# Kernel tuning notes

Hardware: AMD Instinct MI355X
Metric: run time of the kernel (lower is better)

Reference implementation:

```python
import jax, jax.numpy as jnp
import numpy as np

B, C, W, H = 4, 256, 128, 128
BLK = 16
D = C // 8


def setup_inputs() -> dict:
    key = jax.random.key(0)
    ks = jax.random.split(key, 7)
    s = 0.05
    return {
        "x": jax.random.normal(ks[0], (B, C, W, H), jnp.float32),
        "Wq": jax.random.normal(ks[1], (D, C), jnp.float32) * s,
        "bq": jax.random.normal(ks[2], (D,), jnp.float32) * s,
        "Wk": jax.random.normal(ks[3], (D, C), jnp.float32) * s,
        "bk": jax.random.normal(ks[4], (D,), jnp.float32) * s,
        "Wv": jax.random.normal(ks[5], (C, C), jnp.float32) * s,
        "bv": jax.random.normal(ks[6], (C,), jnp.float32) * s,
        "gamma": jnp.full((1,), 0.5, jnp.float32),
    }


def reference(x, Wq, bq, Wk, bk, Wv, bv, gamma):
    Bx, Cx, Wx, Hx = x.shape
    blk = BLK
    pw = (blk - Wx % blk) % blk
    ph = (blk - Hx % blk) % blk
    xp = jnp.pad(x, ((0, 0), (0, 0), (0, pw), (0, ph))) if (pw or ph) else x
    Wp, Hp = xp.shape[2], xp.shape[3]
    nW, nH = Wp // blk, Hp // blk
    N = blk * blk
    # partition into non-overlapping blk x blk windows -> (G, C, N)
    xb = xp.reshape(Bx, Cx, nW, blk, nH, blk).transpose(0, 2, 4, 1, 3, 5)
    xb = xb.reshape(-1, Cx, N)
    # padding mask: positions whose channel-abs-sum is zero are masked out
    mask = jnp.abs(xb).sum(axis=1) > 0  # (G, N) bool
    # 1x1 convs == per-pixel linear projections
    q = jnp.einsum('dc,gcn->gnd', Wq, xb) + bq            # (G, N, D)
    k = jnp.einsum('dc,gcn->gdn', Wk, xb) + bk[:, None]   # (G, D, N)
    energy = jnp.einsum('gnd,gdm->gnm', q, k)             # (G, N, N)
    NEG = jnp.float32(-1e9)
    energy = jnp.where(mask[:, None, :], energy, NEG)  # mask keys
    energy = jnp.where(mask[:, :, None], energy, NEG)  # mask queries
    att = jax.nn.softmax(energy, axis=-1)
    v = jnp.einsum('dc,gcn->gdn', Wv, xb) + bv[:, None]   # (G, C, N)
    out = jnp.einsum('gcm,gnm->gcn', v, att)              # (G, C, N)
    out = out.reshape(Bx, nW, nH, Cx, blk, blk).transpose(0, 3, 1, 4, 2, 5)
    out = out.reshape(Bx, Cx, Wp, Hp)[:, :, :Wx, :Hx]
    out = gamma * out + x
    return out, att
```

## Files before the change

### kernel.cpp

```cpp
#include <hip/hip_runtime.h>

typedef unsigned short u16;
typedef __attribute__((ext_vector_type(8))) short short8;
typedef __attribute__((ext_vector_type(4))) short s16x4;
typedef __attribute__((ext_vector_type(4))) float f32x4;

#define CC 256
#define WW 128
#define HH 128
#define DD 32
#define NN 256
#define WH (WW * HH)
#define P8 524288
#define OUTEL 16777216

__device__ __forceinline__ u16 f2bf(float f) {
  unsigned u = __float_as_uint(f);
  return (u16)((u + 0x7FFFu + ((u >> 16) & 1u)) >> 16);
}
__device__ __forceinline__ float bf2f(u16 h) {
  return __uint_as_float(((unsigned)h) << 16);
}

__global__ __launch_bounds__(256) void k_pack(const float* __restrict__ Wq,
                                              const float* __restrict__ Wk,
                                              float* __restrict__ wqk) {
  int idx = blockIdx.x * 256 + threadIdx.x;
  int r = idx >> 8, c = idx & 255;
  float v = (r < 32) ? Wq[r * 256 + c] : Wk[(r - 32) * 256 + c];
  wqk[c * 64 + r] = v;
}

__global__ __launch_bounds__(1024) void k_qk(const float* __restrict__ x,
                                             const float* __restrict__ wqk,
                                             const float* __restrict__ bq,
                                             const float* __restrict__ bk,
                                             u16* __restrict__ qk) {
  __shared__ float xs[2][64 * 256];
  int hw = blockIdx.x;
  int g = (hw & 7) * 32 + (hw >> 3);
  int bb = g >> 6, wb = (g >> 3) & 7, hb = g & 7;
  int w0 = wb * 16, h0 = hb * 16;
  int t = threadIdx.x, ln = t & 63;
  int dg = __builtin_amdgcn_readfirstlane(t >> 6);
  int dq4 = dg & 7, is_k = dg >> 3;
  const float* xwin = x + (size_t)bb * CC * WH + (size_t)w0 * HH + h0;

  f32x4 st[4];
#pragma unroll
  for (int j = 0; j < 4; ++j) {
    int lin = j * 1024 + t;
    int c = lin >> 6, sub = lin & 63;
    st[j] = *(const f32x4*)(xwin + (size_t)c * WH + (sub >> 2) * HH + (sub & 3) * 4);
  }
#pragma unroll
  for (int j = 0; j < 4; ++j) {
    int lin = j * 1024 + t;
    int c = lin >> 6, sub = lin & 63;
    *(f32x4*)&xs[0][c * 256 + sub * 4] = st[j];
  }

  float acc[4][4];
#pragma unroll
  for (int j = 0; j < 4; ++j)
#pragma unroll
    for (int i = 0; i < 4; ++i) acc[j][i] = 0.f;

  for (int s = 0; s < 4; ++s) {
    int nxt = s + 1;
    if (nxt < 4) {
#pragma unroll
      for (int j = 0; j < 4; ++j) {
        int lin = j * 1024 + t;
        int c = lin >> 6, sub = lin & 63;
        st[j] = *(const f32x4*)(xwin + (size_t)(nxt * 64 + c) * WH + (sub >> 2) * HH +
                                (sub & 3) * 4);
      }
    }
    __syncthreads();
    const float* xb = xs[s & 1];
    const float* wp = wqk + (s * 64) * 64 + dg * 4;
#pragma unroll 4
    for (int cc = 0; cc < 64; ++cc) {
      f32x4 xv = *(const f32x4*)(xb + cc * 256 + 4 * ln);
      f32x4 wv4 = *(const f32x4*)(wp + cc * 64);
#pragma unroll
      for (int j = 0; j < 4; ++j)
#pragma unroll
        for (int i = 0; i < 4; ++i) acc[j][i] = fmaf(wv4[j], xv[i], acc[j][i]);
    }
    if (nxt < 4) {
#pragma unroll
      for (int j = 0; j < 4; ++j) {
        int lin = j * 1024 + t;
        int c = lin >> 6, sub = lin & 63;
        *(f32x4*)&xs[nxt & 1][c * 256 + sub * 4] = st[j];
      }
    }
  }

  const float* bsrc = is_k ? bk : bq;
  float bias[4];
#pragma unroll
  for (int j = 0; j < 4; ++j) bias[j] = bsrc[dq4 * 4 + j];

  u16* ph = qk + ((size_t)((is_k << 3) + (dq4 >> 1))) * P8;
  int sub = (dq4 & 1) * 4;
#pragma unroll
  for (int i = 0; i < 4; ++i) {
    int m = 4 * ln + i;
    s16x4 hv, lv;
#pragma unroll
    for (int j = 0; j < 4; ++j) {
      float v = acc[j][i] + bias[j];
      u16 h = f2bf(v);
      hv[j] = (short)h;
      lv[j] = (short)f2bf(v - bf2f(h));
    }
    size_t ro = (size_t)(g * NN + m) * 8 + sub;
    *(s16x4*)(ph + ro) = hv;
    *(s16x4*)(ph + 4 * (size_t)P8 + ro) = lv;
  }
}

__global__ __launch_bounds__(512, 2) void k_v(const float* __restrict__ x,
                                              const float* __restrict__ Wv,
                                              const float* __restrict__ bv,
                                              u16* __restrict__ vws) {
  __shared__ u16 xb[256 * 44];
  int hw = blockIdx.x;
  int L = (hw & 7) * 64 + (hw >> 3);
  int g = L >> 1, ch = L & 1;
  int bb = g >> 6, wb = (g >> 3) & 7, hb = g & 7;
  int w0 = wb * 16, h0 = hb * 16;
  int t = threadIdx.x, ln = t & 63, wv = t >> 6;
  int cw = wv & 3, mh = wv >> 2;
  int cb = ch * 128 + cw * 32;
  int mb = mh * 128;
  const float* xg = x + (size_t)bb * CC * WH;

  f32x4 acc[2][8];
#pragma unroll
  for (int ci = 0; ci < 2; ++ci)
#pragma unroll
    for (int mt = 0; mt < 8; ++mt) acc[ci][mt] = (f32x4){0.f, 0.f, 0.f, 0.f};

  for (int ks = 0; ks < 8; ++ks) {
    int c0 = ks * 32;
    int q = ln >> 4, cl = wv * 4 + q;
#pragma unroll
    for (int it = 0; it < 4; ++it) {
      int mm = it * 64 + 4 * (ln & 15);
      f32x4 xv = *(const f32x4*)(xg + (size_t)(c0 + cl) * WH + (size_t)(w0 + (mm >> 4)) * HH +
                                 h0 + (mm & 15));
#pragma unroll
      for (int j = 0; j < 4; ++j) xb[(mm + j) * 44 + cl] = f2bf(xv[j]);
    }
    __syncthreads();

    short8 af[2];
#pragma unroll
    for (int ci = 0; ci < 2; ++ci) {
      int row = cb + ci * 16 + (ln & 15);
      const float* wp = Wv + (size_t)row * CC + c0 + (ln >> 4) * 8;
      f32x4 wa = *(const f32x4*)wp;
      f32x4 wb2 = *(const f32x4*)(wp + 4);
#pragma unroll
      for (int j = 0; j < 4; ++j) {
        af[ci][j] = (short)f2bf(wa[j]);
        af[ci][4 + j] = (short)f2bf(wb2[j]);
      }
    }
#pragma unroll
    for (int mt = 0; mt < 8; ++mt) {
      const u16* bp = &xb[(mb + mt * 16 + (ln & 15)) * 44 + (ln >> 4) * 8];
      union { short8 v; s16x4 h[2]; } bu;
      bu.h[0] = *(const s16x4*)bp;
      bu.h[1] = *(const s16x4*)(bp + 4);
#pragma unroll
      for (int ci = 0; ci < 2; ++ci)
        acc[ci][mt] = __builtin_amdgcn_mfma_f32_16x16x32_bf16(af[ci], bu.v, acc[ci][mt], 0, 0, 0);
    }
    __syncthreads();
  }

#pragma unroll
  for (int ci = 0; ci < 2; ++ci)
#pragma unroll
    for (int mt = 0; mt < 8; ++mt)
#pragma unroll
      for (int r = 0; r < 4; ++r) {
        int c = cb + ci * 16 + (ln >> 4) * 4 + r;
        int m = mb + mt * 16 + (ln & 15);
        vws[(size_t)(g * CC + c) * NN + m] = f2bf(acc[ci][mt][r] + bv[c]);
      }
}

__global__ __launch_bounds__(256, 4) void k_attn(const float* __restrict__ x,
                                                 const u16* __restrict__ qk,
                                                 const u16* __restrict__ vws,
                                                 const float* __restrict__ gamma,
                                                 float* __restrict__ dout) {
  __shared__ u16 att_lds[64 * 256];
  int hw = blockIdx.x;
  int L = (hw & 7) * 128 + (hw >> 3);
  int g = L >> 2, qt = L & 3;
  int bb = g >> 6, wb = (g >> 3) & 7, hb = g & 7;
  int w0 = wb * 16, h0 = hb * 16;
  int t = threadIdx.x, ln = t & 63, wv = t >> 6;
  float gam = gamma[0];
  float* attg = dout + (size_t)OUTEL;
  char* smem = (char*)att_lds;
  int n0 = qt * 64;
  int nt = n0 + wv * 16;
  int oct = ln >> 4;

  const u16* qb = qk + (size_t)oct * P8 + (size_t)(g * NN + nt + (ln & 15)) * 8;
  short8 ahi = *(const short8*)qb;
  short8 alo = *(const short8*)(qb + 4 * (size_t)P8);
  f32x4 e[16];
#pragma unroll
  for (int mt = 0; mt < 16; ++mt) e[mt] = (f32x4){0.f, 0.f, 0.f, 0.f};
#pragma unroll
  for (int mt = 0; mt < 16; ++mt) {
    const u16* kb = qk + (size_t)(8 + oct) * P8 + (size_t)(g * NN + mt * 16 + (ln & 15)) * 8;
    short8 bhi = *(const short8*)kb;
    short8 blo = *(const short8*)(kb + 4 * (size_t)P8);
    e[mt] = __builtin_amdgcn_mfma_f32_16x16x32_bf16(ahi, bhi, e[mt], 0, 0, 0);
    e[mt] = __builtin_amdgcn_mfma_f32_16x16x32_bf16(alo, bhi, e[mt], 0, 0, 0);
    e[mt] = __builtin_amdgcn_mfma_f32_16x16x32_bf16(ahi, blo, e[mt], 0, 0, 0);
  }

  float inv[4];
#pragma unroll
  for (int r = 0; r < 4; ++r) {
    float m0 = e[0][r];
#pragma unroll
    for (int mt = 1; mt < 16; ++mt) m0 = fmaxf(m0, e[mt][r]);
    m0 = fmaxf(m0, __shfl_xor(m0, 1));
    m0 = fmaxf(m0, __shfl_xor(m0, 2));
    m0 = fmaxf(m0, __shfl_xor(m0, 4));
    m0 = fmaxf(m0, __shfl_xor(m0, 8));
    float s = 0.f;
#pragma unroll
    for (int mt = 0; mt < 16; ++mt) {
      float p = __expf(e[mt][r] - m0);
      e[mt][r] = p;
      s += p;
    }
    s += __shfl_xor(s, 1);
    s += __shfl_xor(s, 2);
    s += __shfl_xor(s, 4);
    s += __shfl_xor(s, 8);
    inv[r] = 1.0f / s;
  }

#pragma unroll
  for (int mt = 0; mt < 16; ++mt)
#pragma unroll
    for (int r = 0; r < 4; ++r) {
      int nn = wv * 16 + (ln >> 4) * 4 + r;
      int m = mt * 16 + (ln & 15);
      int byteoff = nn * 512 + ((2 * m) ^ ((nn & 7) << 4));
      *(u16*)(smem + byteoff) = f2bf(e[mt][r] * inv[r]);
    }
  __syncthreads();

#pragma unroll
  for (int c = 0; c < 16; ++c) {
    int nn = c * 4 + (t >> 6);
    int m0 = 4 * (t & 63);
    int byteoff = nn * 512 + ((2 * m0) ^ ((nn & 7) << 4));
    s16x4 bv4 = *(const s16x4*)(smem + byteoff);
    f32x4 fv;
#pragma unroll
    for (int j = 0; j < 4; ++j) fv[j] = bf2f((u16)bv4[j]);
    *(f32x4*)(attg + (size_t)(g * NN + n0 + nn) * NN + m0) = fv;
  }

  int cbase = wv * 64;
  f32x4 o[4][4];
#pragma unroll
  for (int ci = 0; ci < 4; ++ci)
#pragma unroll
    for (int ni = 0; ni < 4; ++ni) o[ci][ni] = (f32x4){0.f, 0.f, 0.f, 0.f};

#pragma unroll
  for (int k = 0; k < 8; ++k) {
    short8 a[4];
#pragma unroll
    for (int ci = 0; ci < 4; ++ci)
      a[ci] = *(const short8*)&vws[(size_t)(g * CC + cbase + ci * 16 + (ln & 15)) * NN + k * 32 +
                                   (ln >> 4) * 8];
    short8 bf[4];
#pragma unroll
    for (int ni = 0; ni < 4; ++ni) {
      int nn = ni * 16 + (ln & 15);
      int byteoff = nn * 512 + ((2 * (k * 32 + (ln >> 4) * 8)) ^ ((nn & 7) << 4));
      bf[ni] = *(const short8*)(smem + byteoff);
    }
#pragma unroll
    for (int ci = 0; ci < 4; ++ci)
#pragma unroll
      for (int ni = 0; ni < 4; ++ni)
        o[ci][ni] = __builtin_amdgcn_mfma_f32_16x16x32_bf16(a[ci], bf[ni], o[ci][ni], 0, 0, 0);
  }

#pragma unroll
  for (int ci = 0; ci < 4; ++ci)
#pragma unroll
    for (int ni = 0; ni < 4; ++ni)
#pragma unroll
      for (int r = 0; r < 4; ++r) {
        int c = cbase + ci * 16 + (ln >> 4) * 4 + r;
        int n = n0 + ni * 16 + (ln & 15);
        size_t addr = (size_t)(bb * CC + c) * WH + (size_t)(w0 + (n >> 4)) * HH + h0 + (n & 15);
        dout[addr] = gam * o[ci][ni][r] + x[addr];
      }
}

extern "C" void kernel_launch(void* const* d_in, const int* in_sizes, int n_in,
                              void* d_out, int out_size, void* d_ws, size_t ws_size,
                              hipStream_t stream) {
  const float* x = (const float*)d_in[0];
  const float* Wq = (const float*)d_in[1];
  const float* bq = (const float*)d_in[2];
  const float* Wk = (const float*)d_in[3];
  const float* bk = (const float*)d_in[4];
  const float* Wv = (const float*)d_in[5];
  const float* bv = (const float*)d_in[6];
  const float* gamma = (const float*)d_in[7];
  float* out = (float*)d_out;

  float* wqk = (float*)d_ws;
  u16* qk = (u16*)((char*)d_ws + 65536);
  u16* vws = qk + 16 * (size_t)P8;

  k_pack<<<64, 256, 0, stream>>>(Wq, Wk, wqk);
  k_qk<<<256, 1024, 0, stream>>>(x, wqk, bq, bk, qk);
  k_v<<<512, 512, 0, stream>>>(x, Wv, bv, vws);
  k_attn<<<1024, 256, 0, stream>>>(x, qk, vws, gamma, out);
}
```

Measured before the change: 314.9 us.

## Reassociate value projection after attention and drop separate V kernel

Removes the standalone V-projection kernel. The QK kernel now also writes a bf16 copy of each window of x, and the attention kernel first computes x·attᵀ, stages it in LDS, then multiplies by Wv and adds bias (bias is valid since attention rows sum to one). This trades a kernel launch and the V workspace round-trip for a second MFMA GEMM per attention block plus an extra bf16 rounding of the intermediate.

After: 292.4 us. -7.1%, faster.

```diff
diff --git a/kernel.cpp b/kernel.cpp
--- a/kernel.cpp
+++ b/kernel.cpp
@@ -35,7 +35,8 @@
                                              const float* __restrict__ wqk,
                                              const float* __restrict__ bq,
                                              const float* __restrict__ bk,
-                                             u16* __restrict__ qk) {
+                                             u16* __restrict__ qk,
+                                             u16* __restrict__ xbf) {
   __shared__ float xs[2][64 * 256];
   int hw = blockIdx.x;
   int g = (hw & 7) * 32 + (hw >> 3);
@@ -45,6 +46,7 @@
   int dg = __builtin_amdgcn_readfirstlane(t >> 6);
   int dq4 = dg & 7, is_k = dg >> 3;
   const float* xwin = x + (size_t)bb * CC * WH + (size_t)w0 * HH + h0;
+  u16* xbg = xbf + (size_t)g * CC * NN;
 
   f32x4 st[4];
 #pragma unroll
@@ -58,6 +60,10 @@
     int lin = j * 1024 + t;
     int c = lin >> 6, sub = lin & 63;
     *(f32x4*)&xs[0][c * 256 + sub * 4] = st[j];
+    s16x4 bp;
+#pragma unroll
+    for (int i = 0; i < 4; ++i) bp[i] = (short)f2bf(st[j][i]);
+    *(s16x4*)&xbg[(size_t)c * NN + sub * 4] = bp;
   }
 
   float acc[4][4];
@@ -95,6 +101,10 @@
         int lin = j * 1024 + t;
         int c = lin >> 6, sub = lin & 63;
         *(f32x4*)&xs[nxt & 1][c * 256 + sub * 4] = st[j];
+        s16x4 bp;
+#pragma unroll
+        for (int i = 0; i < 4; ++i) bp[i] = (short)f2bf(st[j][i]);
+        *(s16x4*)&xbg[(size_t)(nxt * 64 + c) * NN + sub * 4] = bp;
       }
     }
   }
@@ -123,85 +133,14 @@
   }
 }
 
-__global__ __launch_bounds__(512, 2) void k_v(const float* __restrict__ x,
-                                              const float* __restrict__ Wv,
-                                              const float* __restrict__ bv,
-                                              u16* __restrict__ vws) {
-  __shared__ u16 xb[256 * 44];
-  int hw = blockIdx.x;
-  int L = (hw & 7) * 64 + (hw >> 3);
-  int g = L >> 1, ch = L & 1;
-  int bb = g >> 6, wb = (g >> 3) & 7, hb = g & 7;
-  int w0 = wb * 16, h0 = hb * 16;
-  int t = threadIdx.x, ln = t & 63, wv = t >> 6;
-  int cw = wv & 3, mh = wv >> 2;
-  int cb = ch * 128 + cw * 32;
-  int mb = mh * 128;
-  const float* xg = x + (size_t)bb * CC * WH;
-
-  f32x4 acc[2][8];
-#pragma unroll
-  for (int ci = 0; ci < 2; ++ci)
-#pragma unroll
-    for (int mt = 0; mt < 8; ++mt) acc[ci][mt] = (f32x4){0.f, 0.f, 0.f, 0.f};
-
-  for (int ks = 0; ks < 8; ++ks) {
-    int c0 = ks * 32;
-    int q = ln >> 4, cl = wv * 4 + q;
-#pragma unroll
-    for (int it = 0; it < 4; ++it) {
-      int mm = it * 64 + 4 * (ln & 15);
-      f32x4 xv = *(const f32x4*)(xg + (size_t)(c0 + cl) * WH + (size_t)(w0 + (mm >> 4)) * HH +
-                                 h0 + (mm & 15));
-#pragma unroll
-      for (int j = 0; j < 4; ++j) xb[(mm + j) * 44 + cl] = f2bf(xv[j]);
-    }
-    __syncthreads();
-
-    short8 af[2];
-#pragma unroll
-    for (int ci = 0; ci < 2; ++ci) {
-      int row = cb + ci * 16 + (ln & 15);
-      const float* wp = Wv + (size_t)row * CC + c0 + (ln >> 4) * 8;
-      f32x4 wa = *(const f32x4*)wp;
-      f32x4 wb2 = *(const f32x4*)(wp + 4);
-#pragma unroll
-      for (int j = 0; j < 4; ++j) {
-        af[ci][j] = (short)f2bf(wa[j]);
-        af[ci][4 + j] = (short)f2bf(wb2[j]);
-      }
-    }
-#pragma unroll
-    for (int mt = 0; mt < 8; ++mt) {
-      const u16* bp = &xb[(mb + mt * 16 + (ln & 15)) * 44 + (ln >> 4) * 8];
-      union { short8 v; s16x4 h[2]; } bu;
-      bu.h[0] = *(const s16x4*)bp;
-      bu.h[1] = *(const s16x4*)(bp + 4);
-#pragma unroll
-      for (int ci = 0; ci < 2; ++ci)
-        acc[ci][mt] = __builtin_amdgcn_mfma_f32_16x16x32_bf16(af[ci], bu.v, acc[ci][mt], 0, 0, 0);
-    }
-    __syncthreads();
-  }
-
-#pragma unroll
-  for (int ci = 0; ci < 2; ++ci)
-#pragma unroll
-    for (int mt = 0; mt < 8; ++mt)
-#pragma unroll
-      for (int r = 0; r < 4; ++r) {
-        int c = cb + ci * 16 + (ln >> 4) * 4 + r;
-        int m = mb + mt * 16 + (ln & 15);
-        vws[(size_t)(g * CC + c) * NN + m] = f2bf(acc[ci][mt][r] + bv[c]);
-      }
-}
-
 __global__ __launch_bounds__(256, 4) void k_attn(const float* __restrict__ x,
+                                                 const float* __restrict__ Wv,
+                                                 const float* __restrict__ bv,
                                                  const u16* __restrict__ qk,
-                                                 const u16* __restrict__ vws,
+                                                 const u16* __restrict__ xbf,
                                                  const float* __restrict__ gamma,
                                                  float* __restrict__ dout) {
-  __shared__ u16 att_lds[64 * 256];
+  __shared__ u16 tile[64 * 256];
   int hw = blockIdx.x;
   int L = (hw & 7) * 128 + (hw >> 3);
   int g = L >> 2, qt = L & 3;
@@ -210,7 +149,7 @@
   int t = threadIdx.x, ln = t & 63, wv = t >> 6;
   float gam = gamma[0];
   float* attg = dout + (size_t)OUTEL;
-  char* smem = (char*)att_lds;
+  char* smem = (char*)tile;
   int n0 = qt * 64;
   int nt = n0 + wv * 16;
   int oct = ln >> 4;
@@ -279,35 +218,86 @@
   }
 
   int cbase = wv * 64;
-  f32x4 o[4][4];
+  const u16* xbg = xbf + (size_t)g * CC * NN;
+  f32x4 y[4][4];
 #pragma unroll
   for (int ci = 0; ci < 4; ++ci)
 #pragma unroll
-    for (int ni = 0; ni < 4; ++ni) o[ci][ni] = (f32x4){0.f, 0.f, 0.f, 0.f};
-
-#pragma unroll
-  for (int k = 0; k < 8; ++k) {
+    for (int ni = 0; ni < 4; ++ni) y[ci][ni] = (f32x4){0.f, 0.f, 0.f, 0.f};
+
+#pragma unroll
+  for (int kk = 0; kk < 8; ++kk) {
     short8 a[4];
 #pragma unroll
     for (int ci = 0; ci < 4; ++ci)
-      a[ci] = *(const short8*)&vws[(size_t)(g * CC + cbase + ci * 16 + (ln & 15)) * NN + k * 32 +
+      a[ci] = *(const short8*)&xbg[(size_t)(cbase + ci * 16 + (ln & 15)) * NN + kk * 32 +
                                    (ln >> 4) * 8];
     short8 bf[4];
 #pragma unroll
     for (int ni = 0; ni < 4; ++ni) {
       int nn = ni * 16 + (ln & 15);
-      int byteoff = nn * 512 + ((2 * (k * 32 + (ln >> 4) * 8)) ^ ((nn & 7) << 4));
+      int byteoff = nn * 512 + ((2 * (kk * 32 + (ln >> 4) * 8)) ^ ((nn & 7) << 4));
       bf[ni] = *(const short8*)(smem + byteoff);
     }
 #pragma unroll
     for (int ci = 0; ci < 4; ++ci)
 #pragma unroll
       for (int ni = 0; ni < 4; ++ni)
-        o[ci][ni] = __builtin_amdgcn_mfma_f32_16x16x32_bf16(a[ci], bf[ni], o[ci][ni], 0, 0, 0);
-  }
+        y[ci][ni] = __builtin_amdgcn_mfma_f32_16x16x32_bf16(a[ci], bf[ni], y[ci][ni], 0, 0, 0);
+  }
+  __syncthreads();
 
 #pragma unroll
   for (int ci = 0; ci < 4; ++ci)
+#pragma unroll
+    for (int ni = 0; ni < 4; ++ni)
+#pragma unroll
+      for (int r = 0; r < 4; ++r) {
+        int nn = ni * 16 + (ln & 15);
+        int cin = cbase + ci * 16 + (ln >> 4) * 4 + r;
+        int byteoff = nn * 512 + ((2 * cin) ^ ((nn & 7) << 4));
+        *(u16*)(smem + byteoff) = f2bf(y[ci][ni][r]);
+      }
+  __syncthreads();
+
+  f32x4 o[4][4];
+#pragma unroll
+  for (int ci = 0; ci < 4; ++ci)
+#pragma unroll
+    for (int ni = 0; ni < 4; ++ni) o[ci][ni] = (f32x4){0.f, 0.f, 0.f, 0.f};
+
+#pragma unroll
+  for (int kk = 0; kk < 8; ++kk) {
+    short8 wf[4];
+#pragma unroll
+    for (int ci = 0; ci < 4; ++ci) {
+      int row = cbase + ci * 16 + (ln & 15);
+      const float* wp = Wv + (size_t)row * CC + kk * 32 + (ln >> 4) * 8;
+      f32x4 wa = *(const f32x4*)wp;
+      f32x4 wb2 = *(const f32x4*)(wp + 4);
+#pragma unroll
+      for (int j = 0; j < 4; ++j) {
+        wf[ci][j] = (short)f2bf(wa[j]);
+        wf[ci][4 + j] = (short)f2bf(wb2[j]);
+      }
+    }
+    short8 bf[4];
+#pragma unroll
+    for (int ni = 0; ni < 4; ++ni) {
+      int nn = ni * 16 + (ln & 15);
+      int byteoff = nn * 512 + ((2 * (kk * 32 + (ln >> 4) * 8)) ^ ((nn & 7) << 4));
+      bf[ni] = *(const short8*)(smem + byteoff);
+    }
+#pragma unroll
+    for (int ci = 0; ci < 4; ++ci)
+#pragma unroll
+      for (int ni = 0; ni < 4; ++ni)
+        o[ci][ni] = __builtin_amdgcn_mfma_f32_16x16x32_bf16(wf[ci], bf[ni], o[ci][ni], 0, 0, 0);
+  }
+
+#pragma unroll
+  for (int ci = 0; ci < 4; ++ci) {
+    f32x4 bvv = *(const f32x4*)(bv + cbase + ci * 16 + (ln >> 4) * 4);
 #pragma unroll
     for (int ni = 0; ni < 4; ++ni)
 #pragma unroll
@@ -315,8 +305,9 @@
         int c = cbase + ci * 16 + (ln >> 4) * 4 + r;
         int n = n0 + ni * 16 + (ln & 15);
         size_t addr = (size_t)(bb * CC + c) * WH + (size_t)(w0 + (n >> 4)) * HH + h0 + (n & 15);
-        dout[addr] = gam * o[ci][ni][r] + x[addr];
-      }
+        dout[addr] = gam * (o[ci][ni][r] + bvv[r]) + x[addr];
+      }
+  }
 }
 
 extern "C" void kernel_launch(void* const* d_in, const int* in_sizes, int n_in,
@@ -334,10 +325,9 @@
 
   float* wqk = (float*)d_ws;
   u16* qk = (u16*)((char*)d_ws + 65536);
-  u16* vws = qk + 16 * (size_t)P8;
+  u16* xbf = qk + 16 * (size_t)P8;
 
   k_pack<<<64, 256, 0, stream>>>(Wq, Wk, wqk);
-  k_qk<<<256, 1024, 0, stream>>>(x, wqk, bq, bk, qk);
-  k_v<<<512, 512, 0, stream>>>(x, Wv, bv, vws);
-  k_attn<<<1024, 256, 0, stream>>>(x, qk, vws, gamma, out);
-}
+  k_qk<<<256, 1024, 0, stream>>>(x, wqk, bq, bk, qk, xbf);
+  k_attn<<<1024, 256, 0, stream>>>(x, Wv, bv, qk, xbf, gamma, out);
+}
```
